# Kernel optimization log

Hardware: AMD Instinct MI355X
Metric: run time of the kernel (lower is better)

## Reference

```python
import jax, jax.numpy as jnp
import numpy as np

N = 50000        # num nodes (hyperedge ids also live in [0, N), matching old PyG quirk)
E = 1600000      # num incidence pairs
F_IN = 512       # input features
HEADS = 8
OUT1 = 8         # hconv1 out_channels per head
HID = HEADS * OUT1  # 64
NCLS = 7
NEG_SLOPE = 0.2


def setup_inputs() -> dict:
    key = jax.random.key(0)
    ks = jax.random.split(key, 8)
    x = jax.random.normal(ks[0], (N, F_IN), dtype=jnp.float32)
    edge_index = jax.random.randint(ks[1], (2, E), 0, N, dtype=jnp.int32)
    hyperedge_weight = jax.random.uniform(ks[2], (N,), dtype=jnp.float32) + 0.1
    W1 = jax.random.normal(ks[3], (F_IN, HEADS * OUT1), dtype=jnp.float32) * (1.0 / np.sqrt(F_IN))
    att1 = jax.random.normal(ks[4], (1, HEADS, 2 * OUT1), dtype=jnp.float32) * 0.1
    b1 = jnp.zeros((HEADS * OUT1,), dtype=jnp.float32)
    W2 = jax.random.normal(ks[5], (HID, NCLS), dtype=jnp.float32) * (1.0 / np.sqrt(HID))
    b2 = jnp.zeros((NCLS,), dtype=jnp.float32)
    return {"x": x, "edge_index": edge_index, "hyperedge_weight": hyperedge_weight,
            "W1": W1, "att1": att1, "b1": b1, "W2": W2, "b2": b2}


def _segment_softmax(a, seg, n):
    # numerically-stable softmax over groups defined by seg (per column / head)
    amax = jax.ops.segment_max(a, seg, num_segments=n)
    amax = jnp.where(jnp.isfinite(amax), amax, 0.0)
    ex = jnp.exp(a - amax[seg])
    den = jax.ops.segment_sum(ex, seg, num_segments=n)
    return ex / (den[seg] + 1e-16)


def _hconv(x, edge_index, hw, W, bias, heads, out_ch, att=None):
    """Old-PyG HypergraphConv forward (dropout disabled / eval mode)."""
    row, col = edge_index[0], edge_index[1]   # row: node ids, col: hyperedge ids
    n = x.shape[0]
    ones = jnp.ones(row.shape[0], dtype=x.dtype)
    xh = (x @ W).reshape(n, heads, out_ch)    # [N, H, C]

    if att is not None:
        # split att to avoid materializing cat([x_i, x_j]) per edge
        s_i = (xh * att[..., :out_ch]).sum(-1)   # [N, H]
        s_j = (xh * att[..., out_ch:]).sum(-1)   # [N, H]
        a = jax.nn.leaky_relu(s_i[row] + s_j[col], NEG_SLOPE)  # [E, H]
        alpha = _segment_softmax(a, row, n)      # grouped by source node
    else:
        alpha = None

    # node degree norm D (weighted by hyperedge weight)
    D = jax.ops.segment_sum(hw[col], row, num_segments=n)
    Dinv = jnp.where(D > 0, 1.0 / D, 0.0)
    # hyperedge degree norm B, scaled by hyperedge weight
    Bdeg = jax.ops.segment_sum(ones, col, num_segments=n)
    Binv = jnp.where(Bdeg > 0, 1.0 / Bdeg, 0.0) * hw

    # propagate 1: nodes -> hyperedges, norm = B[target]
    msg1 = xh[row] * Binv[col][:, None, None]          # [E, H, C]
    if alpha is not None:
        msg1 = msg1 * alpha[:, :, None]
    out_e = jax.ops.segment_sum(msg1, col, num_segments=n)  # [N, H, C]

    # propagate 2: hyperedges -> nodes, norm = D[target]
    msg2 = out_e[col] * Dinv[row][:, None, None]       # [E, H, C]
    if alpha is not None:
        msg2 = msg2 * alpha[:, :, None]
    out = jax.ops.segment_sum(msg2, row, num_segments=n)    # [N, H, C]

    return out.reshape(n, heads * out_ch) + bias   # concat=True


def reference(x, edge_index, hyperedge_weight, W1, att1, b1, W2, b2):
    # eval mode: F.dropout(p=0.6) is identity
    h = jax.nn.elu(_hconv(x, edge_index, hyperedge_weight, W1, b1, HEADS, OUT1, att1))
    out = _hconv(h, edge_index, hyperedge_weight, W2, b2, 1, NCLS, None)
    return jax.nn.log_softmax(out, axis=1)
```

## Files before the change

kernel.cpp:

```cpp
#include <hip/hip_runtime.h>
#include <hip/hip_bf16.h>
#include <cmath>

#define NN    50000
#define EE    1600000
#define FIN   512
#define NHEAD 8
#define OUT1  8
#define HID   64
#define NCLS  7

#define NB    391
#define EPB   4096
#define LOG2E 1.4426950408889634f

#define OFF_P0     0
#define OFF_SJ     3200000
#define OFF_SIRD   3600000
#define OFF_DINV   4400000
#define OFF_BINV   4450000
#define OFF_XH16   4500000
#define OFF_ACCE16 5300000
#define OFF_H      7700000
#define OFF_XH2    10900000
#define OFF_ACCE2  11300000
#define OFF_RPTR   11700000
#define OFF_CPTR   11760000
#define OFF_BHR    11820000
#define OFF_BHC    11821000
#define OFF_BSR    11822000
#define OFF_BSC    11823000
#define OFF_BCR    11824000
#define OFF_BCC    11825000
#define OFF_CSRRC  11830000
#define OFF_CSRCR  12700000

#define LRELU(a) ((a) > 0.f ? (a) : 0.2f * (a))

__device__ __forceinline__ float fexp2(float x) {
#if __has_builtin(__builtin_amdgcn_exp2f)
  return __builtin_amdgcn_exp2f(x);
#else
  return exp2f(x);
#endif
}

__device__ __forceinline__ float bf2f(unsigned short u) {
  union { unsigned int i; float f; } v;
  v.i = ((unsigned int)u) << 16;
  return v.f;
}
__device__ __forceinline__ unsigned short f2bf(float f) {
  union { float f; unsigned int i; } v;
  v.f = f;
  unsigned int r = v.i + 0x7FFFu + ((v.i >> 16) & 1u);
  return (unsigned short)(r >> 16);
}

__global__ __launch_bounds__(512) void zero_small(int* __restrict__ bh_r,
                                                  int* __restrict__ bh_c) {
  int t = threadIdx.x;
  if (t <= NB) { bh_r[t] = 0; bh_c[t] = 0; }
}

__global__ __launch_bounds__(256) void bucket_hist(const int* __restrict__ ei,
                                                   int* __restrict__ bh_r,
                                                   int* __restrict__ bh_c) {
  __shared__ int hr[NB], hc[NB];
  int t = threadIdx.x;
  for (int i = t; i < NB; i += 256) { hr[i] = 0; hc[i] = 0; }
  __syncthreads();
  for (int i = blockIdx.x * 256 + t; i < EE; i += gridDim.x * 256) {
    atomicAdd(hr + (ei[i] >> 7), 1);
    atomicAdd(hc + (ei[EE + i] >> 7), 1);
  }
  __syncthreads();
  for (int i = t; i < NB; i += 256) {
    if (hr[i]) atomicAdd(bh_r + i, hr[i]);
    if (hc[i]) atomicAdd(bh_c + i, hc[i]);
  }
}

__global__ __launch_bounds__(512) void bucket_scan(const int* __restrict__ bh_r,
                                                   const int* __restrict__ bh_c,
                                                   int* __restrict__ bs_r,
                                                   int* __restrict__ bs_c,
                                                   int* __restrict__ bc_r,
                                                   int* __restrict__ bc_c) {
  __shared__ int lds[512];
  int t = threadIdx.x;
  for (int side = 0; side < 2; ++side) {
    const int* bh = side ? bh_c : bh_r;
    int* bs = side ? bs_c : bs_r;
    int* bc = side ? bc_c : bc_r;
    int v = (t < NB) ? bh[t] : 0;
    lds[t] = v;
    __syncthreads();
    for (int off = 1; off < 512; off <<= 1) {
      int u = (t >= off) ? lds[t - off] : 0;
      __syncthreads();
      lds[t] += u;
      __syncthreads();
    }
    int excl = lds[t] - v;
    if (t <= NB) bs[t] = excl;
    if (t < NB) bc[t] = excl;
    __syncthreads();
  }
}

__global__ __launch_bounds__(256) void phaseA(const int* __restrict__ ei,
                                              int* __restrict__ bc_r,
                                              int* __restrict__ bc_c,
                                              int* __restrict__ tmp_r,
                                              int* __restrict__ tmp_c) {
  __shared__ int er[EPB];
  __shared__ int ec[EPB];
  __shared__ int hr[NB], hc[NB];
  const int e0 = blockIdx.x * EPB;
  const int cntE = min(EPB, EE - e0);
  const int t = threadIdx.x;
  for (int i = t; i < cntE; i += 256) { er[i] = ei[e0 + i]; ec[i] = ei[EE + e0 + i]; }
  for (int i = t; i < NB; i += 256) { hr[i] = 0; hc[i] = 0; }
  __syncthreads();
  for (int i = t; i < cntE; i += 256) {
    atomicAdd(hr + (er[i] >> 7), 1);
    atomicAdd(hc + (ec[i] >> 7), 1);
  }
  __syncthreads();
  for (int i = t; i < NB; i += 256) {
    int n = hr[i];
    hr[i] = n ? atomicAdd(bc_r + i, n) : 0;
    n = hc[i];
    hc[i] = n ? atomicAdd(bc_c + i, n) : 0;
  }
  __syncthreads();
  for (int i = t; i < cntE; i += 256) {
    int r = er[i], c = ec[i];
    int pr = atomicAdd(hr + (r >> 7), 1);
    tmp_r[pr] = ((r & 127) << 16) | c;
    int pc = atomicAdd(hc + (c >> 7), 1);
    tmp_c[pc] = ((c & 127) << 16) | r;
  }
}

__global__ __launch_bounds__(256) void phaseB(const int* __restrict__ tmp_r,
                                              const int* __restrict__ tmp_c,
                                              const int* __restrict__ bs_r,
                                              const int* __restrict__ bs_c,
                                              const float* __restrict__ hw,
                                              int* __restrict__ rptr,
                                              int* __restrict__ cptr,
                                              unsigned short* __restrict__ csr_row_c,
                                              unsigned short* __restrict__ csr_col_r,
                                              float* __restrict__ Binv,
                                              float* __restrict__ dinv) {
  const int side = blockIdx.x >= NB ? 1 : 0;
  const int b = blockIdx.x - side * NB;
  const int* tmp = side ? tmp_c : tmp_r;
  const int* bs = side ? bs_c : bs_r;
  int* ptr = side ? cptr : rptr;
  unsigned short* csr = side ? csr_col_r : csr_row_c;

  const int base = bs[b];
  const int M = bs[b + 1] - base;
  __shared__ int cnt[128], pre[128], cur[128];
  __shared__ float ds[128];
  const int t = threadIdx.x;
  if (t < 128) { cnt[t] = 0; ds[t] = 0.f; }
  __syncthreads();
  for (int i = t; i < M; i += 256) atomicAdd(cnt + (tmp[base + i] >> 16), 1);
  __syncthreads();
  if (t < 128) pre[t] = cnt[t];
  __syncthreads();
  for (int off = 1; off < 128; off <<= 1) {
    int u = (t >= off && t < 128) ? pre[t - off] : 0;
    __syncthreads();
    if (t < 128) pre[t] += u;
    __syncthreads();
  }
  const int node0 = b << 7;
  if (t < 128) {
    int excl = pre[t] - cnt[t];
    int g = node0 + t;
    if (g <= NN) ptr[g] = base + excl;
    cur[t] = base + excl;
    if (side && g < NN) Binv[g] = cnt[t] > 0 ? hw[g] / (float)cnt[t] : 0.f;
  }
  __syncthreads();
  for (int i = t; i < M; i += 256) {
    int e = tmp[base + i];
    int own = e >> 16;
    int other = e & 0xFFFF;
    int pos = atomicAdd(cur + own, 1);
    csr[pos] = (unsigned short)other;
    if (!side) atomicAdd(ds + own, hw[other]);
  }
  __syncthreads();
  if (!side && t < 128) {
    int g = node0 + t;
    if (g < NN) dinv[g] = ds[t] > 0.f ? 1.0f / ds[t] : 0.f;
  }
}

__global__ __launch_bounds__(256) void gemm1_kernel(const float* __restrict__ x,
                                                    const float* __restrict__ W1,
                                                    float* __restrict__ p0,
                                                    float* __restrict__ p1) {
  __shared__ float lx[32][66];
  __shared__ float lw[32][68];
  const int t = threadIdx.x;
  const int row0 = blockIdx.x * 64;
  const int kbase = blockIdx.y * (FIN / 2);
  float* __restrict__ dst = blockIdx.y ? p1 : p0;
  const int ty = t >> 4, tx = t & 15;
  const int r0 = ty * 4, c0 = tx * 4;
  const int sr = t >> 2;
  const int sk = (t & 3) * 8;
  const int grow = row0 + sr;
  const int wk = t >> 3;
  const int wc = (t & 7) * 8;

  float acc[4][4] = {};

  for (int kb = kbase; kb < kbase + FIN / 2; kb += 32) {
    {
      float4 a0 = make_float4(0.f, 0.f, 0.f, 0.f), a1 = a0;
      if (grow < NN) {
        const float4* p = reinterpret_cast<const float4*>(x + (size_t)grow * FIN + kb + sk);
        a0 = p[0]; a1 = p[1];
      }
      lx[sk + 0][sr] = a0.x; lx[sk + 1][sr] = a0.y;
      lx[sk + 2][sr] = a0.z; lx[sk + 3][sr] = a0.w;
      lx[sk + 4][sr] = a1.x; lx[sk + 5][sr] = a1.y;
      lx[sk + 6][sr] = a1.z; lx[sk + 7][sr] = a1.w;
    }
    {
      const float4* q = reinterpret_cast<const float4*>(W1 + (size_t)(kb + wk) * HID + wc);
      float4 b0 = q[0], b1v = q[1];
      *reinterpret_cast<float4*>(&lw[wk][wc]) = b0;
      *reinterpret_cast<float4*>(&lw[wk][wc + 4]) = b1v;
    }
    __syncthreads();
#pragma unroll
    for (int kk = 0; kk < 32; ++kk) {
      const float4 af = *reinterpret_cast<const float4*>(&lx[kk][r0]);
      const float4 bf = *reinterpret_cast<const float4*>(&lw[kk][c0]);
      const float a4[4] = {af.x, af.y, af.z, af.w};
      const float b4[4] = {bf.x, bf.y, bf.z, bf.w};
#pragma unroll
      for (int i = 0; i < 4; ++i)
#pragma unroll
        for (int j = 0; j < 4; ++j)
          acc[i][j] = fmaf(a4[i], b4[j], acc[i][j]);
    }
    __syncthreads();
  }
#pragma unroll
  for (int i = 0; i < 4; ++i) {
    int gr = row0 + r0 + i;
    if (gr < NN) {
      float4 v = make_float4(acc[i][0], acc[i][1], acc[i][2], acc[i][3]);
      *reinterpret_cast<float4*>(dst + (size_t)gr * HID + c0) = v;
    }
  }
}

__global__ __launch_bounds__(256) void attscore_kernel(const float* __restrict__ p0,
                                                       const float* __restrict__ p1,
                                                       const float* __restrict__ att1,
                                                       unsigned short* __restrict__ xh16,
                                                       float2* __restrict__ sird,
                                                       float* __restrict__ s_j) {
  int t = blockIdx.x * 256 + threadIdx.x;
  if (t >= NN * NHEAD) return;
  int hh = t & 7;
  const size_t base = (size_t)t * 8;
  float4 a0 = *reinterpret_cast<const float4*>(p0 + base);
  float4 a1 = *reinterpret_cast<const float4*>(p0 + base + 4);
  float4 q0 = *reinterpret_cast<const float4*>(p1 + base);
  float4 q1 = *reinterpret_cast<const float4*>(p1 + base + 4);
  float v[8] = {a0.x + q0.x, a0.y + q0.y, a0.z + q0.z, a0.w + q0.w,
                a1.x + q1.x, a1.y + q1.y, a1.z + q1.z, a1.w + q1.w};
  float si = 0.f, sj = 0.f;
#pragma unroll
  for (int c = 0; c < OUT1; ++c) {
    si = fmaf(v[c], att1[hh * 16 + c], si);
    sj = fmaf(v[c], att1[hh * 16 + 8 + c], sj);
  }
  uint4 packed;
  packed.x = (unsigned int)f2bf(v[0]) | ((unsigned int)f2bf(v[1]) << 16);
  packed.y = (unsigned int)f2bf(v[2]) | ((unsigned int)f2bf(v[3]) << 16);
  packed.z = (unsigned int)f2bf(v[4]) | ((unsigned int)f2bf(v[5]) << 16);
  packed.w = (unsigned int)f2bf(v[6]) | ((unsigned int)f2bf(v[7]) << 16);
  *reinterpret_cast<uint4*>(xh16 + base) = packed;
  sird[t] = make_float2(si * LOG2E, 0.f);
  s_j[t] = sj * LOG2E;
}

__global__ __launch_bounds__(256) void den_csr(const int* __restrict__ rptr,
                                               const unsigned short* __restrict__ csr_row_c,
                                               const float* __restrict__ s_j,
                                               float2* __restrict__ sird) {
  int wid = (blockIdx.x * 256 + threadIdx.x) >> 6;
  int lane = threadIdx.x & 63;
  if (wid >= NN) return;
  int r = wid;
  int hh = lane & 7;
  int eslot = lane >> 3;
  float si = sird[r * 8 + hh].x;
  int beg = rptr[r], end = rptr[r + 1];
  float aexp = 0.f;
  int i = beg + eslot;
  for (; i + 8 < end; i += 16) {
    int c0 = csr_row_c[i], c1 = csr_row_c[i + 8];
    float sj0 = s_j[c0 * 8 + hh], sj1 = s_j[c1 * 8 + hh];
    float a0 = LRELU(si + sj0), a1 = LRELU(si + sj1);
    aexp += fexp2(a0) + fexp2(a1);
  }
  if (i < end) {
    int c = csr_row_c[i];
    float a = LRELU(si + s_j[c * 8 + hh]);
    aexp += fexp2(a);
  }
  aexp += __shfl_xor(aexp, 8);
  aexp += __shfl_xor(aexp, 16);
  aexp += __shfl_xor(aexp, 32);
  if (eslot == 0)
    reinterpret_cast<float*>(sird)[(r * 8 + hh) * 2 + 1] = 1.0f / (aexp + 1e-16f);
}

__global__ __launch_bounds__(256) void prop1_csr(const int* __restrict__ cptr,
                                                 const unsigned short* __restrict__ csr_col_r,
                                                 const unsigned short* __restrict__ xh16,
                                                 const float2* __restrict__ sird,
                                                 const float* __restrict__ s_j,
                                                 const float* __restrict__ Binv,
                                                 unsigned short* __restrict__ acc_e16) {
  int wid = (blockIdx.x * 256 + threadIdx.x) >> 6;
  int lane = threadIdx.x & 63;
  if (wid >= NN) return;
  const int c = wid;
  const int hh = lane >> 3;
  const int j = lane & 7;
  const int abase = lane & 56;
  float sj = s_j[c * 8 + hh];
  int beg = cptr[c], end = cptr[c + 1];
  float acc = 0.f;
  int i = beg;
  for (; i + 16 <= end; i += 16) {
    int r0 = csr_col_r[i + j];
    int r1 = csr_col_r[i + 8 + j];
    float2 q0 = sird[r0 * 8 + hh];
    float2 q1 = sird[r1 * 8 + hh];
    unsigned short va[8], vb[8];
#pragma unroll
    for (int j2 = 0; j2 < 8; ++j2)
      va[j2] = xh16[(__shfl(r0, j2) << 6) + lane];
#pragma unroll
    for (int j2 = 0; j2 < 8; ++j2)
      vb[j2] = xh16[(__shfl(r1, j2) << 6) + lane];
    float a0 = fexp2(LRELU(q0.x + sj)) * q0.y;
    float a1 = fexp2(LRELU(q1.x + sj)) * q1.y;
#pragma unroll
    for (int j2 = 0; j2 < 8; ++j2)
      acc = fmaf(bf2f(va[j2]), __shfl(a0, abase + j2), acc);
#pragma unroll
    for (int j2 = 0; j2 < 8; ++j2)
      acc = fmaf(bf2f(vb[j2]), __shfl(a1, abase + j2), acc);
  }
  for (; i + 8 <= end; i += 8) {
    int rj = csr_col_r[i + j];
    float2 q = sird[rj * 8 + hh];
    unsigned short va[8];
#pragma unroll
    for (int j2 = 0; j2 < 8; ++j2)
      va[j2] = xh16[(__shfl(rj, j2) << 6) + lane];
    float aexp = fexp2(LRELU(q.x + sj)) * q.y;
#pragma unroll
    for (int j2 = 0; j2 < 8; ++j2)
      acc = fmaf(bf2f(va[j2]), __shfl(aexp, abase + j2), acc);
  }
  for (; i < end; ++i) {
    int r = csr_col_r[i];
    float2 q = sird[r * 8 + hh];
    float a = LRELU(q.x + sj);
    acc = fmaf(bf2f(xh16[(r << 6) + lane]), fexp2(a) * q.y, acc);
  }
  acc_e16[(c << 6) + lane] = f2bf(acc * Binv[c]);
}

__global__ __launch_bounds__(256) void prop2_csr(const int* __restrict__ rptr,
                                                 const unsigned short* __restrict__ csr_row_c,
                                                 const unsigned short* __restrict__ acc_e16,
                                                 const float2* __restrict__ sird,
                                                 const float* __restrict__ s_j,
                                                 const float* __restrict__ dinv,
                                                 const float* __restrict__ b1,
                                                 float* __restrict__ h) {
  int wid = (blockIdx.x * 256 + threadIdx.x) >> 6;
  int lane = threadIdx.x & 63;
  if (wid >= NN) return;
  const int r = wid;
  const int hh = lane >> 3;
  const int j = lane & 7;
  const int abase = lane & 56;
  float2 sr = sird[r * 8 + hh];
  const float si = sr.x, rd = sr.y;
  int beg = rptr[r], end = rptr[r + 1];
  float acc = 0.f;
  int i = beg;
  for (; i + 16 <= end; i += 16) {
    int c0 = csr_row_c[i + j];
    int c1 = csr_row_c[i + 8 + j];
    float sj0 = s_j[c0 * 8 + hh];
    float sj1 = s_j[c1 * 8 + hh];
    unsigned short va[8], vb[8];
#pragma unroll
    for (int j2 = 0; j2 < 8; ++j2)
      va[j2] = acc_e16[(__shfl(c0, j2) << 6) + lane];
#pragma unroll
    for (int j2 = 0; j2 < 8; ++j2)
      vb[j2] = acc_e16[(__shfl(c1, j2) << 6) + lane];
    float a0 = fexp2(LRELU(si + sj0));
    float a1 = fexp2(LRELU(si + sj1));
#pragma unroll
    for (int j2 = 0; j2 < 8; ++j2)
      acc = fmaf(bf2f(va[j2]), __shfl(a0, abase + j2), acc);
#pragma unroll
    for (int j2 = 0; j2 < 8; ++j2)
      acc = fmaf(bf2f(vb[j2]), __shfl(a1, abase + j2), acc);
  }
  for (; i + 8 <= end; i += 8) {
    int cj = csr_row_c[i + j];
    float sjv = s_j[cj * 8 + hh];
    unsigned short va[8];
#pragma unroll
    for (int j2 = 0; j2 < 8; ++j2)
      va[j2] = acc_e16[(__shfl(cj, j2) << 6) + lane];
    float aexp = fexp2(LRELU(si + sjv));
#pragma unroll
    for (int j2 = 0; j2 < 8; ++j2)
      acc = fmaf(bf2f(va[j2]), __shfl(aexp, abase + j2), acc);
  }
  for (; i < end; ++i) {
    int cc = csr_row_c[i];
    float aexp = fexp2(LRELU(si + s_j[cc * 8 + hh]));
    acc = fmaf(bf2f(acc_e16[(cc << 6) + lane]), aexp, acc);
  }
  acc *= rd;
  float v = fmaf(acc, dinv[r], b1[lane]);
  h[(r << 6) + lane] = v > 0.f ? v : expm1f(v);
}

__global__ __launch_bounds__(256) void gemm2_kernel(const float* __restrict__ h,
                                                    const float* __restrict__ W2,
                                                    float* __restrict__ xh2) {
  int t = blockIdx.x * 256 + threadIdx.x;
  if (t >= NN * 8) return;
  int n = t >> 3, k = t & 7;
  if (k == 7) { xh2[t] = 0.f; return; }
  const float* hp = h + (size_t)n * HID;
  float acc = 0.f;
#pragma unroll
  for (int c = 0; c < HID; ++c) acc = fmaf(hp[c], W2[c * NCLS + k], acc);
  xh2[t] = acc;
}

__global__ __launch_bounds__(256) void prop3_csr(const int* __restrict__ cptr,
                                                 const unsigned short* __restrict__ csr_col_r,
                                                 const float* __restrict__ xh2,
                                                 const float* __restrict__ Binv,
                                                 float* __restrict__ acc_e2) {
  int t = blockIdx.x * 256 + threadIdx.x;
  int g = t >> 3, k = t & 7;
  if (g >= NN) return;
  int beg = cptr[g], end = cptr[g + 1];
  float acc = 0.f;
  int i = beg;
  for (; i + 3 < end; i += 4) {
    int r0 = csr_col_r[i], r1 = csr_col_r[i + 1];
    int r2 = csr_col_r[i + 2], r3 = csr_col_r[i + 3];
    float v0 = xh2[r0 * 8 + k], v1 = xh2[r1 * 8 + k];
    float v2 = xh2[r2 * 8 + k], v3 = xh2[r3 * 8 + k];
    acc += (v0 + v1) + (v2 + v3);
  }
  for (; i < end; ++i) acc += xh2[csr_col_r[i] * 8 + k];
  acc_e2[g * 8 + k] = acc * Binv[g];
}

__global__ __launch_bounds__(256) void prop4_csr(const int* __restrict__ rptr,
                                                 const unsigned short* __restrict__ csr_row_c,
                                                 const float* __restrict__ acc_e2,
                                                 const float* __restrict__ dinv,
                                                 const float* __restrict__ b2,
                                                 float* __restrict__ out) {
  int t = blockIdx.x * 256 + threadIdx.x;
  int r = t >> 3, k = t & 7;
  if (r >= NN) return;
  int beg = rptr[r], end = rptr[r + 1];
  float acc = 0.f;
  int i = beg;
  for (; i + 3 < end; i += 4) {
    int c0 = csr_row_c[i], c1 = csr_row_c[i + 1];
    int c2 = csr_row_c[i + 2], c3 = csr_row_c[i + 3];
    float v0 = acc_e2[c0 * 8 + k], v1 = acc_e2[c1 * 8 + k];
    float v2 = acc_e2[c2 * 8 + k], v3 = acc_e2[c3 * 8 + k];
    acc += (v0 + v1) + (v2 + v3);
  }
  for (; i < end; ++i) acc += acc_e2[csr_row_c[i] * 8 + k];
  float v = (k < NCLS) ? fmaf(acc, dinv[r], b2[k]) : -INFINITY;
  float m = v;
  m = fmaxf(m, __shfl_xor(m, 1, 8));
  m = fmaxf(m, __shfl_xor(m, 2, 8));
  m = fmaxf(m, __shfl_xor(m, 4, 8));
  float ex = (k < NCLS) ? expf(v - m) : 0.f;
  float s = ex;
  s += __shfl_xor(s, 1, 8);
  s += __shfl_xor(s, 2, 8);
  s += __shfl_xor(s, 4, 8);
  float lse = m + logf(s);
  if (k < NCLS) out[(size_t)r * NCLS + k] = v - lse;
}

extern "C" void kernel_launch(void* const* d_in, const int* in_sizes, int n_in,
                              void* d_out, int out_size, void* d_ws, size_t ws_size,
                              hipStream_t stream) {
  const float* x    = (const float*)d_in[0];
  const int*   ei   = (const int*)d_in[1];
  const float* hw   = (const float*)d_in[2];
  const float* W1   = (const float*)d_in[3];
  const float* att1 = (const float*)d_in[4];
  const float* b1   = (const float*)d_in[5];
  const float* W2   = (const float*)d_in[6];
  const float* b2   = (const float*)d_in[7];
  float* out = (float*)d_out;
  float* ws  = (float*)d_ws;

  float* p0buf  = ws + OFF_P0;
  float* s_j    = ws + OFF_SJ;
  float2* sird  = (float2*)(ws + OFF_SIRD);
  float* dinv   = ws + OFF_DINV;
  float* Binv   = ws + OFF_BINV;
  unsigned short* xh16    = (unsigned short*)(ws + OFF_XH16);
  unsigned short* acc_e16 = (unsigned short*)(ws + OFF_ACCE16);
  float* hbuf   = ws + OFF_H;
  float* xh2    = ws + OFF_XH2;
  float* acc_e2 = ws + OFF_ACCE2;
  int* rptr = (int*)(ws + OFF_RPTR);
  int* cptr = (int*)(ws + OFF_CPTR);
  int* bh_r = (int*)(ws + OFF_BHR);
  int* bh_c = (int*)(ws + OFF_BHC);
  int* bs_r = (int*)(ws + OFF_BSR);
  int* bs_c = (int*)(ws + OFF_BSC);
  int* bc_r = (int*)(ws + OFF_BCR);
  int* bc_c = (int*)(ws + OFF_BCC);
  unsigned short* csr_row_c = (unsigned short*)(ws + OFF_CSRRC);
  unsigned short* csr_col_r = (unsigned short*)(ws + OFF_CSRCR);
  int* tmp_r = (int*)(ws + OFF_P0);
  int* tmp_c = (int*)(ws + OFF_XH16);

  zero_small<<<1, 512, 0, stream>>>(bh_r, bh_c);
  bucket_hist<<<256, 256, 0, stream>>>(ei, bh_r, bh_c);
  bucket_scan<<<1, 512, 0, stream>>>(bh_r, bh_c, bs_r, bs_c, bc_r, bc_c);
  phaseA<<<(EE + EPB - 1) / EPB, 256, 0, stream>>>(ei, bc_r, bc_c, tmp_r, tmp_c);
  phaseB<<<2 * NB, 256, 0, stream>>>(tmp_r, tmp_c, bs_r, bs_c, hw,
                                     rptr, cptr, csr_row_c, csr_col_r, Binv, dinv);

  {
    dim3 g((NN + 63) / 64, 2);
    gemm1_kernel<<<g, 256, 0, stream>>>(x, W1, p0buf, hbuf);
  }
  attscore_kernel<<<(NN * NHEAD + 255) / 256, 256, 0, stream>>>(p0buf, hbuf, att1,
                                                                xh16, sird, s_j);
  den_csr<<<(NN * 64 + 255) / 256, 256, 0, stream>>>(rptr, csr_row_c, s_j, sird);
  prop1_csr<<<(NN * 64 + 255) / 256, 256, 0, stream>>>(cptr, csr_col_r, xh16, sird,
                                                       s_j, Binv, acc_e16);
  prop2_csr<<<(NN * 64 + 255) / 256, 256, 0, stream>>>(rptr, csr_row_c, acc_e16, sird,
                                                       s_j, dinv, b1, hbuf);

  gemm2_kernel<<<(NN * 8 + 255) / 256, 256, 0, stream>>>(hbuf, W2, xh2);
  prop3_csr<<<(NN * 8 + 255) / 256, 256, 0, stream>>>(cptr, csr_col_r, xh2, Binv, acc_e2);
  prop4_csr<<<(NN * 8 + 255) / 256, 256, 0, stream>>>(rptr, csr_row_c, acc_e2, dinv, b2, out);
}
```

Measured before the change: 318.9 us.

## Use bf16 MFMA for first GEMM and drop split-K partial buffers

Replaces the fp32 FMA tiled GEMM (split-K into two partial buffers summed later) with a bf16 MFMA 16x16x32 kernel that reads fp32 x, converts it to bf16 in LDS, and writes bf16 xh directly. A new small kernel pre-transposes W1 into bf16. The attention-score kernel now reads the bf16 xh instead of summing two fp32 partials, which removes large intermediate traffic. The cost is lower precision in the GEMM inputs (bf16 x and W1) and an extra launch. The w1t buffer aliases hbuf, which is safe only because hbuf is written later, in prop2.

```diff
diff --git a/kernel.cpp b/kernel.cpp
--- a/kernel.cpp
+++ b/kernel.cpp
@@ -37,6 +37,9 @@
 
 #define LRELU(a) ((a) > 0.f ? (a) : 0.2f * (a))
 
+typedef __attribute__((ext_vector_type(8))) short bf16x8;
+typedef __attribute__((ext_vector_type(4))) float f32x4;
+
 __device__ __forceinline__ float fexp2(float x) {
 #if __has_builtin(__builtin_amdgcn_exp2f)
   return __builtin_amdgcn_exp2f(x);
@@ -61,6 +64,14 @@
                                                   int* __restrict__ bh_c) {
   int t = threadIdx.x;
   if (t <= NB) { bh_r[t] = 0; bh_c[t] = 0; }
+}
+
+__global__ __launch_bounds__(256) void wconv_kernel(const float* __restrict__ W1,
+                                                    unsigned short* __restrict__ w1t) {
+  int idx = blockIdx.x * 256 + threadIdx.x;
+  if (idx >= FIN * HID) return;
+  int k = idx >> 6, col = idx & 63;
+  w1t[col * FIN + k] = f2bf(W1[idx]);
 }
 
 __global__ __launch_bounds__(256) void bucket_hist(const int* __restrict__ ei,
@@ -203,97 +214,83 @@
   }
 }
 
-__global__ __launch_bounds__(256) void gemm1_kernel(const float* __restrict__ x,
-                                                    const float* __restrict__ W1,
-                                                    float* __restrict__ p0,
-                                                    float* __restrict__ p1) {
-  __shared__ float lx[32][66];
-  __shared__ float lw[32][68];
+__global__ __launch_bounds__(256) void gemm1_mfma(const float* __restrict__ x,
+                                                  const unsigned short* __restrict__ w1t,
+                                                  unsigned short* __restrict__ xh16) {
+  __shared__ unsigned short lxA[64][40];
+  __shared__ unsigned short lwB[64][40];
   const int t = threadIdx.x;
+  const int w = t >> 6;
+  const int lane = t & 63;
   const int row0 = blockIdx.x * 64;
-  const int kbase = blockIdx.y * (FIN / 2);
-  float* __restrict__ dst = blockIdx.y ? p1 : p0;
-  const int ty = t >> 4, tx = t & 15;
-  const int r0 = ty * 4, c0 = tx * 4;
   const int sr = t >> 2;
   const int sk = (t & 3) * 8;
-  const int grow = row0 + sr;
-  const int wk = t >> 3;
-  const int wc = (t & 7) * 8;
-
-  float acc[4][4] = {};
-
-  for (int kb = kbase; kb < kbase + FIN / 2; kb += 32) {
+  const int fr = lane & 15;
+  const int fk = (lane >> 4) * 8;
+
+  f32x4 acc[4] = {f32x4{0.f, 0.f, 0.f, 0.f}, f32x4{0.f, 0.f, 0.f, 0.f},
+                  f32x4{0.f, 0.f, 0.f, 0.f}, f32x4{0.f, 0.f, 0.f, 0.f}};
+
+  for (int kb = 0; kb < FIN; kb += 32) {
     {
+      int grow = row0 + sr;
       float4 a0 = make_float4(0.f, 0.f, 0.f, 0.f), a1 = a0;
       if (grow < NN) {
         const float4* p = reinterpret_cast<const float4*>(x + (size_t)grow * FIN + kb + sk);
         a0 = p[0]; a1 = p[1];
       }
-      lx[sk + 0][sr] = a0.x; lx[sk + 1][sr] = a0.y;
-      lx[sk + 2][sr] = a0.z; lx[sk + 3][sr] = a0.w;
-      lx[sk + 4][sr] = a1.x; lx[sk + 5][sr] = a1.y;
-      lx[sk + 6][sr] = a1.z; lx[sk + 7][sr] = a1.w;
+      uint4 packed;
+      packed.x = (unsigned int)f2bf(a0.x) | ((unsigned int)f2bf(a0.y) << 16);
+      packed.y = (unsigned int)f2bf(a0.z) | ((unsigned int)f2bf(a0.w) << 16);
+      packed.z = (unsigned int)f2bf(a1.x) | ((unsigned int)f2bf(a1.y) << 16);
+      packed.w = (unsigned int)f2bf(a1.z) | ((unsigned int)f2bf(a1.w) << 16);
+      *reinterpret_cast<uint4*>(&lxA[sr][sk]) = packed;
     }
     {
-      const float4* q = reinterpret_cast<const float4*>(W1 + (size_t)(kb + wk) * HID + wc);
-      float4 b0 = q[0], b1v = q[1];
-      *reinterpret_cast<float4*>(&lw[wk][wc]) = b0;
-      *reinterpret_cast<float4*>(&lw[wk][wc + 4]) = b1v;
+      const uint4* q = reinterpret_cast<const uint4*>(w1t + (size_t)sr * FIN + kb + sk);
+      *reinterpret_cast<uint4*>(&lwB[sr][sk]) = q[0];
     }
     __syncthreads();
-#pragma unroll
-    for (int kk = 0; kk < 32; ++kk) {
-      const float4 af = *reinterpret_cast<const float4*>(&lx[kk][r0]);
-      const float4 bf = *reinterpret_cast<const float4*>(&lw[kk][c0]);
-      const float a4[4] = {af.x, af.y, af.z, af.w};
-      const float b4[4] = {bf.x, bf.y, bf.z, bf.w};
-#pragma unroll
-      for (int i = 0; i < 4; ++i)
-#pragma unroll
-        for (int j = 0; j < 4; ++j)
-          acc[i][j] = fmaf(a4[i], b4[j], acc[i][j]);
+    bf16x8 afrag = *reinterpret_cast<const bf16x8*>(&lxA[16 * w + fr][fk]);
+#pragma unroll
+    for (int b = 0; b < 4; ++b) {
+      bf16x8 bfrag = *reinterpret_cast<const bf16x8*>(&lwB[16 * b + fr][fk]);
+      acc[b] = __builtin_amdgcn_mfma_f32_16x16x32_bf16(afrag, bfrag, acc[b], 0, 0, 0);
     }
     __syncthreads();
   }
-#pragma unroll
-  for (int i = 0; i < 4; ++i) {
-    int gr = row0 + r0 + i;
+  const int crow0 = row0 + 16 * w + (lane >> 4) * 4;
+#pragma unroll
+  for (int v = 0; v < 4; ++v) {
+    int gr = crow0 + v;
     if (gr < NN) {
-      float4 v = make_float4(acc[i][0], acc[i][1], acc[i][2], acc[i][3]);
-      *reinterpret_cast<float4*>(dst + (size_t)gr * HID + c0) = v;
+#pragma unroll
+      for (int b = 0; b < 4; ++b)
+        xh16[(size_t)gr * HID + 16 * b + fr] = f2bf(acc[b][v]);
     }
   }
 }
 
-__global__ __launch_bounds__(256) void attscore_kernel(const float* __restrict__ p0,
-                                                       const float* __restrict__ p1,
+__global__ __launch_bounds__(256) void attscore_kernel(const unsigned short* __restrict__ xh16,
                                                        const float* __restrict__ att1,
-                                                       unsigned short* __restrict__ xh16,
                                                        float2* __restrict__ sird,
                                                        float* __restrict__ s_j) {
   int t = blockIdx.x * 256 + threadIdx.x;
   if (t >= NN * NHEAD) return;
   int hh = t & 7;
   const size_t base = (size_t)t * 8;
-  float4 a0 = *reinterpret_cast<const float4*>(p0 + base);
-  float4 a1 = *reinterpret_cast<const float4*>(p0 + base + 4);
-  float4 q0 = *reinterpret_cast<const float4*>(p1 + base);
-  float4 q1 = *reinterpret_cast<const float4*>(p1 + base + 4);
-  float v[8] = {a0.x + q0.x, a0.y + q0.y, a0.z + q0.z, a0.w + q0.w,
-                a1.x + q1.x, a1.y + q1.y, a1.z + q1.z, a1.w + q1.w};
+  uint4 p = *reinterpret_cast<const uint4*>(xh16 + base);
+  float v[8];
+  v[0] = bf2f((unsigned short)(p.x & 0xFFFF)); v[1] = bf2f((unsigned short)(p.x >> 16));
+  v[2] = bf2f((unsigned short)(p.y & 0xFFFF)); v[3] = bf2f((unsigned short)(p.y >> 16));
+  v[4] = bf2f((unsigned short)(p.z & 0xFFFF)); v[5] = bf2f((unsigned short)(p.z >> 16));
+  v[6] = bf2f((unsigned short)(p.w & 0xFFFF)); v[7] = bf2f((unsigned short)(p.w >> 16));
   float si = 0.f, sj = 0.f;
 #pragma unroll
   for (int c = 0; c < OUT1; ++c) {
     si = fmaf(v[c], att1[hh * 16 + c], si);
     sj = fmaf(v[c], att1[hh * 16 + 8 + c], sj);
   }
-  uint4 packed;
-  packed.x = (unsigned int)f2bf(v[0]) | ((unsigned int)f2bf(v[1]) << 16);
-  packed.y = (unsigned int)f2bf(v[2]) | ((unsigned int)f2bf(v[3]) << 16);
-  packed.z = (unsigned int)f2bf(v[4]) | ((unsigned int)f2bf(v[5]) << 16);
-  packed.w = (unsigned int)f2bf(v[6]) | ((unsigned int)f2bf(v[7]) << 16);
-  *reinterpret_cast<uint4*>(xh16 + base) = packed;
   sird[t] = make_float2(si * LOG2E, 0.f);
   s_j[t] = sj * LOG2E;
 }
@@ -537,7 +534,6 @@
   float* out = (float*)d_out;
   float* ws  = (float*)d_ws;
 
-  float* p0buf  = ws + OFF_P0;
   float* s_j    = ws + OFF_SJ;
   float2* sird  = (float2*)(ws + OFF_SIRD);
   float* dinv   = ws + OFF_DINV;
@@ -545,6 +541,7 @@
   unsigned short* xh16    = (unsigned short*)(ws + OFF_XH16);
   unsigned short* acc_e16 = (unsigned short*)(ws + OFF_ACCE16);
   float* hbuf   = ws + OFF_H;
+  unsigned short* w1t = (unsigned short*)(ws + OFF_H);
   float* xh2    = ws + OFF_XH2;
   float* acc_e2 = ws + OFF_ACCE2;
   int* rptr = (int*)(ws + OFF_RPTR);
@@ -561,18 +558,15 @@
   int* tmp_c = (int*)(ws + OFF_XH16);
 
   zero_small<<<1, 512, 0, stream>>>(bh_r, bh_c);
+  wconv_kernel<<<(FIN * HID + 255) / 256, 256, 0, stream>>>(W1, w1t);
   bucket_hist<<<256, 256, 0, stream>>>(ei, bh_r, bh_c);
   bucket_scan<<<1, 512, 0, stream>>>(bh_r, bh_c, bs_r, bs_c, bc_r, bc_c);
   phaseA<<<(EE + EPB - 1) / EPB, 256, 0, stream>>>(ei, bc_r, bc_c, tmp_r, tmp_c);
   phaseB<<<2 * NB, 256, 0, stream>>>(tmp_r, tmp_c, bs_r, bs_c, hw,
                                      rptr, cptr, csr_row_c, csr_col_r, Binv, dinv);
 
-  {
-    dim3 g((NN + 63) / 64, 2);
-    gemm1_kernel<<<g, 256, 0, stream>>>(x, W1, p0buf, hbuf);
-  }
-  attscore_kernel<<<(NN * NHEAD + 255) / 256, 256, 0, stream>>>(p0buf, hbuf, att1,
-                                                                xh16, sird, s_j);
+  gemm1_mfma<<<(NN + 63) / 64, 256, 0, stream>>>(x, w1t, xh16);
+  attscore_kernel<<<(NN * NHEAD + 255) / 256, 256, 0, stream>>>(xh16, att1, sird, s_j);
   den_csr<<<(NN * 64 + 255) / 256, 256, 0, stream>>>(rptr, csr_row_c, s_j, sird);
   prop1_csr<<<(NN * 64 + 255) / 256, 256, 0, stream>>>(cptr, csr_col_r, xh16, sird,
                                                        s_j, Binv, acc_e16);
```

Measured after the change: 284.9 us. 1.12x faster.
